# Kernel tuning notes

Hardware: AMD Instinct MI355X
Metric: run time of the kernel (lower is better)

Reference implementation:

```python
import jax, jax.numpy as jnp
import numpy as np

S = 8192
Q_PARAM = 256
V_PARAM = 256
SCALE = 1.0 / np.sqrt(float(Q_PARAM)).astype(np.float32)


def setup_inputs() -> dict:
    key = jax.random.key(0)
    ks = jax.random.split(key, 12)
    init = lambda k, shape, fan_in: jax.random.uniform(k, shape, jnp.float32, -1.0, 1.0) / np.sqrt(float(fan_in))
    return {
        "query": jax.random.normal(ks[0], (S, Q_PARAM), jnp.float32),
        "key": jax.random.normal(ks[1], (S, Q_PARAM), jnp.float32),
        "value": jax.random.normal(ks[2], (S, V_PARAM), jnp.float32),
        "mask": jax.random.uniform(ks[3], (S, S), jnp.float32),
        "Wq": init(ks[4], (Q_PARAM, Q_PARAM), Q_PARAM),
        "bq": init(ks[5], (Q_PARAM,), Q_PARAM),
        "Wk": init(ks[6], (Q_PARAM, Q_PARAM), Q_PARAM),
        "bk": init(ks[7], (Q_PARAM,), Q_PARAM),
        "Wv": init(ks[8], (V_PARAM, V_PARAM), V_PARAM),
        "bv": init(ks[9], (V_PARAM,), V_PARAM),
        "Wo": init(ks[10], (V_PARAM, V_PARAM), V_PARAM),
        "bo": init(ks[11], (V_PARAM,), V_PARAM),
    }


def reference(query, key, value, mask, Wq, bq, Wk, bk, Wv, bv, Wo, bo):
    # torch nn.Linear: y = x @ W.T + b
    q = query @ Wq.T + bq          # [S, q]
    k = key @ Wk.T + bk            # [S, q]
    v = value @ Wv.T + bv          # [S, v]
    scores = q @ k.T               # [S, S]
    masked = scores * mask         # multiplicative mask BEFORE softmax
    h = jax.nn.softmax(masked * SCALE, axis=1)
    h = h @ v                      # [S, v]
    return h @ Wo.T + bo
```

## Files before the change

kernel.cpp:

```cpp
#include <hip/hip_runtime.h>


#define S 8192
#define NSPLIT 8
#define BM 128
#define BN 32
#define KSPL (S / NSPLIT)
#define NT (KSPL / BN)

typedef unsigned short ushort_t;
typedef __attribute__((ext_vector_type(8))) __bf16 bf16x8;
typedef __attribute__((ext_vector_type(4))) float f32x4;
typedef __attribute__((ext_vector_type(4))) ushort_t ushort4_t;
typedef __attribute__((ext_vector_type(8))) ushort_t ushort8_t;
typedef __attribute__((ext_vector_type(4))) unsigned uint4_t;

typedef const __attribute__((address_space(1))) unsigned int* gas_u32;
typedef __attribute__((address_space(3))) unsigned int* las_u32;

__device__ __forceinline__ ushort_t f2bf(float f) {
  unsigned u = __builtin_bit_cast(unsigned, f);
  u += 0x7FFFu + ((u >> 16) & 1u);
  return (ushort_t)(u >> 16);
}

__device__ __forceinline__ bf16x8 pack8(f32x4 a, f32x4 b) {
  ushort8_t u;
  u[0] = f2bf(a[0]); u[1] = f2bf(a[1]); u[2] = f2bf(a[2]); u[3] = f2bf(a[3]);
  u[4] = f2bf(b[0]); u[5] = f2bf(b[1]); u[6] = f2bf(b[2]); u[7] = f2bf(b[3]);
  return __builtin_bit_cast(bf16x8, u);
}

__device__ __forceinline__ unsigned cvt_pk_bf16(float lo, float hi) {
  unsigned r;
  asm("v_cvt_pk_bf16_f32 %0, %1, %2" : "=v"(r) : "v"(lo), "v"(hi));
  return r;
}

__global__ __launch_bounds__(256) void wconv_kernel(
    const float* __restrict__ w0, const float* __restrict__ w1,
    const float* __restrict__ w2, const float* __restrict__ w3,
    ushort_t* __restrict__ o0, ushort_t* __restrict__ o1,
    ushort_t* __restrict__ o2, ushort_t* __restrict__ o3) {
  const int m = blockIdx.y;
  const float* w = (m == 0) ? w0 : (m == 1) ? w1 : (m == 2) ? w2 : w3;
  ushort_t* o = (m == 0) ? o0 : (m == 1) ? o1 : (m == 2) ? o2 : o3;
  const int idx = (blockIdx.x * 256 + threadIdx.x) * 4;
  f32x4 v = *(const f32x4*)(w + idx);
  ushort4_t p;
  p[0] = f2bf(v[0]); p[1] = f2bf(v[1]); p[2] = f2bf(v[2]); p[3] = f2bf(v[3]);
  *(ushort4_t*)(o + idx) = p;
}

__global__ __launch_bounds__(256) void qkv_kernel(
    const float* __restrict__ query, const float* __restrict__ key,
    const float* __restrict__ value,
    const ushort_t* __restrict__ Wqb, const ushort_t* __restrict__ Wkb,
    const ushort_t* __restrict__ Wvb,
    const float* __restrict__ bq, const float* __restrict__ bk,
    const float* __restrict__ bv,
    ushort_t* __restrict__ qo, ushort_t* __restrict__ ko,
    ushort_t* __restrict__ vto) {
  __shared__ __align__(16) ushort_t tb[64 * 68];
  const int z = blockIdx.z;
  const float* inp = (z == 0) ? query : (z == 1) ? key : value;
  const ushort_t* Wb = (z == 0) ? Wqb : (z == 1) ? Wkb : Wvb;
  const float* bias = (z == 0) ? bq : (z == 1) ? bk : bv;

  const int tid = threadIdx.x;
  const int lane = tid & 63;
  const int w = tid >> 6;
  const int lr = lane & 15, lg = lane >> 4;
  const int brow0 = blockIdx.x * 64;
  const int row0 = brow0 + w * 16;
  const int col0 = blockIdx.y * 64;

  f32x4 acc[4] = {};
  const int arow = row0 + lr;
  const int kb = lg * 8;

  bf16x8 af[8];
#pragma unroll
  for (int ks = 0; ks < 8; ++ks) {
    const float* ap = inp + (size_t)arow * 256 + ks * 32 + kb;
    af[ks] = pack8(*(const f32x4*)ap, *(const f32x4*)(ap + 4));
  }
#pragma unroll
  for (int ks = 0; ks < 8; ++ks) {
#pragma unroll
    for (int n = 0; n < 4; ++n) {
      bf16x8 bb = *(const bf16x8*)(Wb + (size_t)(col0 + 16 * n + lr) * 256 + ks * 32 + kb);
      acc[n] = __builtin_amdgcn_mfma_f32_16x16x32_bf16(af[ks], bb, acc[n], 0, 0, 0);
    }
  }

  if (z < 2) {
    ushort_t* o = z ? ko : qo;
#pragma unroll
    for (int n = 0; n < 4; ++n) {
      const int col = col0 + 16 * n + lr;
      const float bv_ = bias[col];
      const int rbase = row0 + lg * 4;
#pragma unroll
      for (int r = 0; r < 4; ++r)
        o[(size_t)(rbase + r) * 256 + col] = f2bf(acc[n][r] + bv_);
    }
  } else {
#pragma unroll
    for (int n = 0; n < 4; ++n) {
      const int col = col0 + 16 * n + lr;
      const float bv_ = bias[col];
      const int cl = 16 * n + lr;
      const int rowl = w * 16 + lg * 4;
      ushort4_t pk;
#pragma unroll
      for (int r = 0; r < 4; ++r) pk[r] = f2bf(acc[n][r] + bv_);
      *(ushort4_t*)&tb[cl * 68 + rowl] = pk;
    }
    __syncthreads();
#pragma unroll
    for (int i = 0; i < 4; ++i) {
      int chunk = i * 256 + tid;
      int c = chunk >> 4;
      int off = (chunk & 15) * 4;
      ushort4_t v0 = *(const ushort4_t*)&tb[c * 68 + off];
      *(ushort4_t*)(vto + (size_t)(col0 + c) * S + brow0 + off) = v0;
    }
  }
}

__global__ __launch_bounds__(256) void oproj_kernel(const ushort_t* __restrict__ inp,
                                                    const ushort_t* __restrict__ Wb,
                                                    const float* __restrict__ bias,
                                                    float* __restrict__ outp) {
  const int tid = threadIdx.x;
  const int lane = tid & 63;
  const int w = tid >> 6;
  const int lr = lane & 15, lg = lane >> 4;
  const int row0 = blockIdx.x * 64 + w * 16;
  const int col0 = blockIdx.y * 64;

  f32x4 acc[4] = {};
  const int arow = row0 + lr;
  const int kb = lg * 8;
#pragma unroll
  for (int ks = 0; ks < 8; ++ks) {
    bf16x8 a = *(const bf16x8*)(inp + (size_t)arow * 256 + ks * 32 + kb);
#pragma unroll
    for (int n = 0; n < 4; ++n) {
      bf16x8 bb = *(const bf16x8*)(Wb + (size_t)(col0 + 16 * n + lr) * 256 + ks * 32 + kb);
      acc[n] = __builtin_amdgcn_mfma_f32_16x16x32_bf16(a, bb, acc[n], 0, 0, 0);
    }
  }
#pragma unroll
  for (int n = 0; n < 4; ++n) {
    const int col = col0 + 16 * n + lr;
    const float bv = bias[col];
    const int rbase = row0 + lg * 4;
#pragma unroll
    for (int r = 0; r < 4; ++r)
      outp[(size_t)(rbase + r) * 256 + col] = acc[n][r] + bv;
  }
}

__global__ __launch_bounds__(256, 2) void flash_kernel(
    const ushort_t* __restrict__ qg, const ushort_t* __restrict__ kbm,
    const ushort_t* __restrict__ vtb, const float* __restrict__ mask,
    float* __restrict__ Opart, float* __restrict__ lpart) {
  __shared__ __align__(16) ushort_t kt[2][BN * 256];
  __shared__ __align__(16) ushort_t vt[2][256 * BN];

  const int tid = threadIdx.x;
  const int lane = tid & 63;
  const int w = tid >> 6;
  const int lr = lane & 15, lg = lane >> 4;
  const int b = blockIdx.x;
  const int split = b & 7;
  const int qx = b >> 3;
  const int kvbase = split * KSPL;
  const int qrow0 = qx * BM + w * 32;

  bf16x8 qf[2][8];
#pragma unroll
  for (int qb = 0; qb < 2; ++qb)
#pragma unroll
    for (int ks = 0; ks < 8; ++ks)
      qf[qb][ks] = *(const bf16x8*)(qg + (size_t)(qrow0 + qb * 16 + lr) * 256 + ks * 32 + lg * 8);

  const float* mrow[2];
#pragma unroll
  for (int qb = 0; qb < 2; ++qb)
    mrow[qb] = mask + (size_t)(qrow0 + qb * 16 + lr) * S + lg * 4;

  f32x4 oacc[2][16] = {};
  float lsum[2] = {0.f, 0.f};
  const int vt_swz = ((lg ^ (lr & 3)) << 4);

  auto stage = [&](int bi, int kv0) {
#pragma unroll
    for (int it = 0; it < 4; ++it) {
      int chunk = it * 256 + (w << 6) + lane;
      int r = chunk >> 5;
      int c = (chunk & 31) ^ (r & 7);
      const ushort_t* src = kbm + (size_t)(kv0 + r) * 256 + c * 8;
      __builtin_amdgcn_global_load_lds((gas_u32)src,
                                       (las_u32)(&kt[bi][0] + it * 2048 + w * 512), 16, 0, 0);
    }
#pragma unroll
    for (int it = 0; it < 4; ++it) {
      int chunk = it * 256 + (w << 6) + lane;
      int r = chunk >> 2;
      int c = (chunk & 3) ^ (r & 3);
      const ushort_t* src = vtb + (size_t)r * S + kv0 + c * 8;
      __builtin_amdgcn_global_load_lds((gas_u32)src,
                                       (las_u32)(&vt[bi][0] + it * 2048 + w * 512), 16, 0, 0);
    }
  };

  f32x4 mcur[2][2];
  auto ld_mask = [&](int kv0) {
#pragma unroll
    for (int qb = 0; qb < 2; ++qb)
#pragma unroll
      for (int kb = 0; kb < 2; ++kb)
        mcur[qb][kb] = __builtin_nontemporal_load((const f32x4*)(mrow[qb] + kv0 + kb * 16));
  };

  stage(0, kvbase);
  ld_mask(kvbase);
  asm volatile("s_waitcnt vmcnt(4)" ::: "memory");
  __builtin_amdgcn_s_barrier();
  __builtin_amdgcn_sched_barrier(0);

  for (int t = 0; t < NT; ++t) {
    const int cur = t & 1;
    const int kvn = kvbase + ((t + 1 < NT) ? (t + 1) : t) * BN;

    stage(cur ^ 1, kvn);

    f32x4 sacc[2][2] = {};
    __builtin_amdgcn_s_setprio(1);
#pragma unroll
    for (int ks = 0; ks < 8; ++ks)
#pragma unroll
      for (int kb = 0; kb < 2; ++kb) {
        int addr = ((kb * 16 + lr) << 9) + ((((ks << 2) + lg) ^ (lr & 7)) << 4);
        bf16x8 kf = *(const bf16x8*)((const char*)&kt[cur][0] + addr);
        sacc[0][kb] = __builtin_amdgcn_mfma_f32_16x16x32_bf16(kf, qf[0][ks], sacc[0][kb], 0, 0, 0);
        sacc[1][kb] = __builtin_amdgcn_mfma_f32_16x16x32_bf16(kf, qf[1][ks], sacc[1][kb], 0, 0, 0);
      }
    __builtin_amdgcn_s_setprio(0);

    unsigned pw[2][2][2];
#pragma unroll
    for (int qb = 0; qb < 2; ++qb) {
      float p[8];
#pragma unroll
      for (int kb = 0; kb < 2; ++kb)
#pragma unroll
        for (int r = 0; r < 4; ++r) {
          float pv = __builtin_amdgcn_exp2f(sacc[qb][kb][r] * (mcur[qb][kb][r] * 0.09016844005556021f));
          p[kb * 4 + r] = pv;
          lsum[qb] += pv;
        }
      pw[qb][0][0] = cvt_pk_bf16(p[0], p[1]);
      pw[qb][0][1] = cvt_pk_bf16(p[2], p[3]);
      pw[qb][1][0] = cvt_pk_bf16(p[4], p[5]);
      pw[qb][1][1] = cvt_pk_bf16(p[6], p[7]);
    }

    ld_mask(kvn);

    bf16x8 pfrag[2];
#pragma unroll
    for (int qb = 0; qb < 2; ++qb) {
      unsigned a0 = pw[qb][0][0], a1 = pw[qb][0][1];
      unsigned b0 = pw[qb][1][0], b1 = pw[qb][1][1];
      asm("v_permlane32_swap_b32 %0, %1" : "+v"(a0), "+v"(b0));
      asm("v_permlane16_swap_b32 %0, %1" : "+v"(a0), "+v"(b0));
      asm("v_permlane32_swap_b32 %0, %1" : "+v"(a1), "+v"(b1));
      asm("v_permlane16_swap_b32 %0, %1" : "+v"(a1), "+v"(b1));
      uint4_t u = {a0, a1, b0, b1};
      pfrag[qb] = __builtin_bit_cast(bf16x8, u);
    }

    __builtin_amdgcn_s_setprio(1);
#pragma unroll
    for (int nd = 0; nd < 16; ++nd) {
      bf16x8 va = *(const bf16x8*)((const char*)&vt[cur][0] + nd * 1024 + lr * 64 + vt_swz);
      oacc[0][nd] = __builtin_amdgcn_mfma_f32_16x16x32_bf16(va, pfrag[0], oacc[0][nd], 0, 0, 0);
      oacc[1][nd] = __builtin_amdgcn_mfma_f32_16x16x32_bf16(va, pfrag[1], oacc[1][nd], 0, 0, 0);
    }
    __builtin_amdgcn_s_setprio(0);

    asm volatile("s_waitcnt vmcnt(4)" ::: "memory");
    __builtin_amdgcn_s_barrier();
    __builtin_amdgcn_sched_barrier(0);
  }

#pragma unroll
  for (int qb = 0; qb < 2; ++qb) {
    float v = lsum[qb];
    v += __shfl_xor(v, 16);
    v += __shfl_xor(v, 32);
    if (lane < 16)
      lpart[(size_t)split * S + qrow0 + qb * 16 + lr] = v;
#pragma unroll
    for (int nd = 0; nd < 16; ++nd)
      *(f32x4*)(Opart + ((size_t)split * S + qrow0 + qb * 16 + lr) * 256 + nd * 16 + lg * 4) = oacc[qb][nd];
  }
}

__global__ __launch_bounds__(256) void combine_kernel(const float* __restrict__ Opart,
                                                      const float* __restrict__ lpart,
                                                      ushort_t* __restrict__ hb) {
  const size_t idx = ((size_t)blockIdx.x * 256 + threadIdx.x) * 4;
  const int row = (int)(idx >> 8);
  float L = 0.f;
  f32x4 acc = {};
#pragma unroll
  for (int s2 = 0; s2 < NSPLIT; ++s2) {
    L += lpart[(size_t)s2 * S + row];
    f32x4 v = *(const f32x4*)(Opart + (size_t)s2 * S * 256 + idx);
    acc[0] += v[0]; acc[1] += v[1]; acc[2] += v[2]; acc[3] += v[3];
  }
  const float inv = 1.0f / L;
  ushort4_t p;
  p[0] = f2bf(acc[0] * inv); p[1] = f2bf(acc[1] * inv);
  p[2] = f2bf(acc[2] * inv); p[3] = f2bf(acc[3] * inv);
  *(ushort4_t*)(hb + idx) = p;
}

extern "C" void kernel_launch(void* const* d_in, const int* in_sizes, int n_in,
                              void* d_out, int out_size, void* d_ws, size_t ws_size,
                              hipStream_t stream) {
  const float* query = (const float*)d_in[0];
  const float* key   = (const float*)d_in[1];
  const float* value = (const float*)d_in[2];
  const float* mask  = (const float*)d_in[3];
  const float* Wq = (const float*)d_in[4];
  const float* bq = (const float*)d_in[5];
  const float* Wk = (const float*)d_in[6];
  const float* bk = (const float*)d_in[7];
  const float* Wv = (const float*)d_in[8];
  const float* bv = (const float*)d_in[9];
  const float* Wo = (const float*)d_in[10];
  const float* bo = (const float*)d_in[11];

  char* ws = (char*)d_ws;
  ushort_t* qb  = (ushort_t*)(ws);
  ushort_t* kb  = (ushort_t*)(ws + ((size_t)4  << 20));
  ushort_t* vtb = (ushort_t*)(ws + ((size_t)8  << 20));
  ushort_t* hb  = (ushort_t*)(ws + ((size_t)12 << 20));
  ushort_t* Wqb = (ushort_t*)(ws + ((size_t)16 << 20));
  ushort_t* Wkb = (ushort_t*)(ws + ((size_t)16 << 20) + (128u << 10));
  ushort_t* Wvb = (ushort_t*)(ws + ((size_t)16 << 20) + (256u << 10));
  ushort_t* Wob = (ushort_t*)(ws + ((size_t)16 << 20) + (384u << 10));
  float* lpart  = (float*)(ws + ((size_t)16 << 20) + (512u << 10));
  float* Opart  = (float*)(ws + ((size_t)17 << 20));

  wconv_kernel<<<dim3(64, 4), 256, 0, stream>>>(Wq, Wk, Wv, Wo, Wqb, Wkb, Wvb, Wob);

  qkv_kernel<<<dim3(S / 64, 4, 3), 256, 0, stream>>>(query, key, value,
                                                     Wqb, Wkb, Wvb, bq, bk, bv,
                                                     qb, kb, vtb);

  flash_kernel<<<dim3(512), 256, 0, stream>>>(qb, kb, vtb, mask, Opart, lpart);

  combine_kernel<<<dim3(S * 256 / 1024), 256, 0, stream>>>(Opart, lpart, hb);

  oproj_kernel<<<dim3(S / 64, 4), 256, 0, stream>>>(hb, Wob, bo, (float*)d_out);
}
```

Baseline: 226.6 us.

## Fuse split-combine into output projection, widen QKV tiles, halve KV splits

```diff
diff --git a/kernel.cpp b/kernel.cpp
--- a/kernel.cpp
+++ b/kernel.cpp
@@ -2,7 +2,7 @@
 
 
 #define S 8192
-#define NSPLIT 8
+#define NSPLIT 4
 #define BM 128
 #define BN 32
 #define KSPL (S / NSPLIT)
@@ -62,7 +62,7 @@
     ushort_t* __restrict__ qo, ushort_t* __restrict__ ko,
     ushort_t* __restrict__ vto) {
   __shared__ __align__(16) ushort_t tb[64 * 68];
-  const int z = blockIdx.z;
+  const int z = blockIdx.y;
   const float* inp = (z == 0) ? query : (z == 1) ? key : value;
   const ushort_t* Wb = (z == 0) ? Wqb : (z == 1) ? Wkb : Wvb;
   const float* bias = (z == 0) ? bq : (z == 1) ? bk : bv;
@@ -73,9 +73,7 @@
   const int lr = lane & 15, lg = lane >> 4;
   const int brow0 = blockIdx.x * 64;
   const int row0 = brow0 + w * 16;
-  const int col0 = blockIdx.y * 64;
-
-  f32x4 acc[4] = {};
+
   const int arow = row0 + lr;
   const int kb = lg * 8;
 
@@ -85,11 +83,13 @@
     const float* ap = inp + (size_t)arow * 256 + ks * 32 + kb;
     af[ks] = pack8(*(const f32x4*)ap, *(const f32x4*)(ap + 4));
   }
+
+  f32x4 acc[16] = {};
 #pragma unroll
   for (int ks = 0; ks < 8; ++ks) {
 #pragma unroll
-    for (int n = 0; n < 4; ++n) {
-      bf16x8 bb = *(const bf16x8*)(Wb + (size_t)(col0 + 16 * n + lr) * 256 + ks * 32 + kb);
+    for (int n = 0; n < 16; ++n) {
+      bf16x8 bb = *(const bf16x8*)(Wb + (size_t)(16 * n + lr) * 256 + ks * 32 + kb);
       acc[n] = __builtin_amdgcn_mfma_f32_16x16x32_bf16(af[ks], bb, acc[n], 0, 0, 0);
     }
   }
@@ -97,8 +97,8 @@
   if (z < 2) {
     ushort_t* o = z ? ko : qo;
 #pragma unroll
-    for (int n = 0; n < 4; ++n) {
-      const int col = col0 + 16 * n + lr;
+    for (int n = 0; n < 16; ++n) {
+      const int col = 16 * n + lr;
       const float bv_ = bias[col];
       const int rbase = row0 + lg * 4;
 #pragma unroll
@@ -106,60 +106,31 @@
         o[(size_t)(rbase + r) * 256 + col] = f2bf(acc[n][r] + bv_);
     }
   } else {
-#pragma unroll
-    for (int n = 0; n < 4; ++n) {
-      const int col = col0 + 16 * n + lr;
-      const float bv_ = bias[col];
-      const int cl = 16 * n + lr;
-      const int rowl = w * 16 + lg * 4;
-      ushort4_t pk;
-#pragma unroll
-      for (int r = 0; r < 4; ++r) pk[r] = f2bf(acc[n][r] + bv_);
-      *(ushort4_t*)&tb[cl * 68 + rowl] = pk;
-    }
-    __syncthreads();
-#pragma unroll
-    for (int i = 0; i < 4; ++i) {
-      int chunk = i * 256 + tid;
-      int c = chunk >> 4;
-      int off = (chunk & 15) * 4;
-      ushort4_t v0 = *(const ushort4_t*)&tb[c * 68 + off];
-      *(ushort4_t*)(vto + (size_t)(col0 + c) * S + brow0 + off) = v0;
-    }
-  }
-}
-
-__global__ __launch_bounds__(256) void oproj_kernel(const ushort_t* __restrict__ inp,
-                                                    const ushort_t* __restrict__ Wb,
-                                                    const float* __restrict__ bias,
-                                                    float* __restrict__ outp) {
-  const int tid = threadIdx.x;
-  const int lane = tid & 63;
-  const int w = tid >> 6;
-  const int lr = lane & 15, lg = lane >> 4;
-  const int row0 = blockIdx.x * 64 + w * 16;
-  const int col0 = blockIdx.y * 64;
-
-  f32x4 acc[4] = {};
-  const int arow = row0 + lr;
-  const int kb = lg * 8;
-#pragma unroll
-  for (int ks = 0; ks < 8; ++ks) {
-    bf16x8 a = *(const bf16x8*)(inp + (size_t)arow * 256 + ks * 32 + kb);
-#pragma unroll
-    for (int n = 0; n < 4; ++n) {
-      bf16x8 bb = *(const bf16x8*)(Wb + (size_t)(col0 + 16 * n + lr) * 256 + ks * 32 + kb);
-      acc[n] = __builtin_amdgcn_mfma_f32_16x16x32_bf16(a, bb, acc[n], 0, 0, 0);
-    }
-  }
-#pragma unroll
-  for (int n = 0; n < 4; ++n) {
-    const int col = col0 + 16 * n + lr;
-    const float bv = bias[col];
-    const int rbase = row0 + lg * 4;
-#pragma unroll
-    for (int r = 0; r < 4; ++r)
-      outp[(size_t)(rbase + r) * 256 + col] = acc[n][r] + bv;
+#pragma unroll 1
+    for (int cb = 0; cb < 4; ++cb) {
+#pragma unroll
+      for (int nn = 0; nn < 4; ++nn) {
+        const int n = cb * 4 + nn;
+        const int col = 16 * n + lr;
+        const float bv_ = bias[col];
+        const int cl = 16 * nn + lr;
+        const int rowl = w * 16 + lg * 4;
+        ushort4_t pk;
+#pragma unroll
+        for (int r = 0; r < 4; ++r) pk[r] = f2bf(acc[n][r] + bv_);
+        *(ushort4_t*)&tb[cl * 68 + rowl] = pk;
+      }
+      __syncthreads();
+#pragma unroll
+      for (int i = 0; i < 4; ++i) {
+        int chunk = i * 256 + tid;
+        int c = chunk >> 4;
+        int off = (chunk & 15) * 4;
+        ushort4_t v0 = *(const ushort4_t*)&tb[c * 68 + off];
+        *(ushort4_t*)(vto + (size_t)(cb * 64 + c) * S + brow0 + off) = v0;
+      }
+      __syncthreads();
+    }
   }
 }
 
@@ -175,8 +146,8 @@
   const int w = tid >> 6;
   const int lr = lane & 15, lg = lane >> 4;
   const int b = blockIdx.x;
-  const int split = b & 7;
-  const int qx = b >> 3;
+  const int split = b & 3;
+  const int qx = b >> 2;
   const int kvbase = split * KSPL;
   const int qrow0 = qx * BM + w * 32;
 
@@ -311,24 +282,62 @@
   }
 }
 
-__global__ __launch_bounds__(256) void combine_kernel(const float* __restrict__ Opart,
-                                                      const float* __restrict__ lpart,
-                                                      ushort_t* __restrict__ hb) {
-  const size_t idx = ((size_t)blockIdx.x * 256 + threadIdx.x) * 4;
-  const int row = (int)(idx >> 8);
-  float L = 0.f;
-  f32x4 acc = {};
-#pragma unroll
-  for (int s2 = 0; s2 < NSPLIT; ++s2) {
-    L += lpart[(size_t)s2 * S + row];
-    f32x4 v = *(const f32x4*)(Opart + (size_t)s2 * S * 256 + idx);
-    acc[0] += v[0]; acc[1] += v[1]; acc[2] += v[2]; acc[3] += v[3];
-  }
-  const float inv = 1.0f / L;
-  ushort4_t p;
-  p[0] = f2bf(acc[0] * inv); p[1] = f2bf(acc[1] * inv);
-  p[2] = f2bf(acc[2] * inv); p[3] = f2bf(acc[3] * inv);
-  *(ushort4_t*)(hb + idx) = p;
+__global__ __launch_bounds__(256) void fuseout_kernel(
+    const float* __restrict__ Opart, const float* __restrict__ lpart,
+    const ushort_t* __restrict__ Wb, const float* __restrict__ bias,
+    float* __restrict__ outp) {
+  __shared__ __align__(16) ushort_t hl[64 * 272];
+
+  const int tid = threadIdx.x;
+  const int lane = tid & 63;
+  const int w = tid >> 6;
+  const int lr = lane & 15, lg = lane >> 4;
+  const int brow0 = blockIdx.x * 64;
+
+#pragma unroll
+  for (int ch = 0; ch < 16; ++ch) {
+    const int e = ch * 1024 + tid * 4;
+    const int row = e >> 8, col = e & 255;
+    float L = 0.f;
+    f32x4 acc = {};
+#pragma unroll
+    for (int s2 = 0; s2 < NSPLIT; ++s2) {
+      L += lpart[(size_t)s2 * S + brow0 + row];
+      f32x4 v = *(const f32x4*)(Opart + ((size_t)s2 * S + brow0 + row) * 256 + col);
+      acc[0] += v[0]; acc[1] += v[1]; acc[2] += v[2]; acc[3] += v[3];
+    }
+    const float inv = 1.0f / L;
+    ushort4_t p;
+    p[0] = f2bf(acc[0] * inv); p[1] = f2bf(acc[1] * inv);
+    p[2] = f2bf(acc[2] * inv); p[3] = f2bf(acc[3] * inv);
+    *(ushort4_t*)&hl[row * 272 + col] = p;
+  }
+  __syncthreads();
+
+  bf16x8 af[8];
+#pragma unroll
+  for (int ks = 0; ks < 8; ++ks)
+    af[ks] = *(const bf16x8*)&hl[(w * 16 + lr) * 272 + ks * 32 + lg * 8];
+
+  f32x4 acc[16] = {};
+#pragma unroll
+  for (int ks = 0; ks < 8; ++ks) {
+#pragma unroll
+    for (int n = 0; n < 16; ++n) {
+      bf16x8 bb = *(const bf16x8*)(Wb + (size_t)(16 * n + lr) * 256 + ks * 32 + lg * 8);
+      acc[n] = __builtin_amdgcn_mfma_f32_16x16x32_bf16(af[ks], bb, acc[n], 0, 0, 0);
+    }
+  }
+
+#pragma unroll
+  for (int n = 0; n < 16; ++n) {
+    const int col = 16 * n + lr;
+    const float bv = bias[col];
+    const int rbase = brow0 + w * 16 + lg * 4;
+#pragma unroll
+    for (int r = 0; r < 4; ++r)
+      outp[(size_t)(rbase + r) * 256 + col] = acc[n][r] + bv;
+  }
 }
 
 extern "C" void kernel_launch(void* const* d_in, const int* in_sizes, int n_in,
@@ -351,23 +360,20 @@
   ushort_t* qb  = (ushort_t*)(ws);
   ushort_t* kb  = (ushort_t*)(ws + ((size_t)4  << 20));
   ushort_t* vtb = (ushort_t*)(ws + ((size_t)8  << 20));
-  ushort_t* hb  = (ushort_t*)(ws + ((size_t)12 << 20));
-  ushort_t* Wqb = (ushort_t*)(ws + ((size_t)16 << 20));
-  ushort_t* Wkb = (ushort_t*)(ws + ((size_t)16 << 20) + (128u << 10));
-  ushort_t* Wvb = (ushort_t*)(ws + ((size_t)16 << 20) + (256u << 10));
-  ushort_t* Wob = (ushort_t*)(ws + ((size_t)16 << 20) + (384u << 10));
-  float* lpart  = (float*)(ws + ((size_t)16 << 20) + (512u << 10));
-  float* Opart  = (float*)(ws + ((size_t)17 << 20));
+  ushort_t* Wqb = (ushort_t*)(ws + ((size_t)12 << 20));
+  ushort_t* Wkb = (ushort_t*)(ws + ((size_t)12 << 20) + (128u << 10));
+  ushort_t* Wvb = (ushort_t*)(ws + ((size_t)12 << 20) + (256u << 10));
+  ushort_t* Wob = (ushort_t*)(ws + ((size_t)12 << 20) + (384u << 10));
+  float* lpart  = (float*)(ws + ((size_t)12 << 20) + (512u << 10));
+  float* Opart  = (float*)(ws + ((size_t)13 << 20));
 
   wconv_kernel<<<dim3(64, 4), 256, 0, stream>>>(Wq, Wk, Wv, Wo, Wqb, Wkb, Wvb, Wob);
 
-  qkv_kernel<<<dim3(S / 64, 4, 3), 256, 0, stream>>>(query, key, value,
-                                                     Wqb, Wkb, Wvb, bq, bk, bv,
-                                                     qb, kb, vtb);
-
-  flash_kernel<<<dim3(512), 256, 0, stream>>>(qb, kb, vtb, mask, Opart, lpart);
-
-  combine_kernel<<<dim3(S * 256 / 1024), 256, 0, stream>>>(Opart, lpart, hb);
-
-  oproj_kernel<<<dim3(S / 64, 4), 256, 0, stream>>>(hb, Wob, bo, (float*)d_out);
-}
+  qkv_kernel<<<dim3(S / 64, 3), 256, 0, stream>>>(query, key, value,
+                                                  Wqb, Wkb, Wvb, bq, bk, bv,
+                                                  qb, kb, vtb);
+
+  flash_kernel<<<dim3(S / BM * NSPLIT), 256, 0, stream>>>(qb, kb, vtb, mask, Opart, lpart);
+
+  fuseout_kernel<<<dim3(S / 64), 256, 0, stream>>>(Opart, lpart, Wob, bo, (float*)d_out);
+}
```

Measured after the change: 305.8 us. +34.9%, slower.
